# Kernel optimization log

Hardware: AMD Instinct MI355X
Metric: run time of the kernel (lower is better)

## Reference

```python
import jax, jax.numpy as jnp
import numpy as np

D, H = 256, 4            # model dim, num heads
HD = D // H              # head dim (even, needed by rotate_half)
B, N, M, NS = 2, 6, 512, 512  # batch, views, t keypoints, s keypoints
EPS = 1e-5


def _linear(x, w, b):
    return x @ w + b


def _ln(x, g, b):
    mu = x.mean(-1, keepdims=True)
    var = ((x - mu) ** 2).mean(-1, keepdims=True)
    return (x - mu) * jax.lax.rsqrt(var + EPS) * g + b


def _ffn(x, f1w, f1b, lng, lnb, f2w, f2b):
    # Linear(2d,2d) -> LayerNorm -> exact GELU -> Linear(2d,d)
    h = jax.nn.gelu(_ln(_linear(x, f1w, f1b), lng, lnb), approximate=False)
    return _linear(h, f2w, f2b)


def _rotate_half(x):
    # pairs (x0,x1) -> (-x1, x0), interleaved
    return jnp.stack((-x[..., 1::2], x[..., 0::2]), axis=-1).reshape(x.shape)


def _rope(freqs, t):
    return t * freqs[0] + _rotate_half(t) * freqs[1]


def _attn(q, k, v):
    sim = jnp.einsum('...id,...jd->...ij', q, k) * (q.shape[-1] ** -0.5)
    return jnp.einsum('...ij,...jd->...id', jax.nn.softmax(sim, axis=-1), v)


def _self_block(x, enc, qkv_w, qkv_b, out_w, out_b, *ffn_p):
    b, n_img, m, d = x.shape
    enc = jnp.swapaxes(enc, 2, 3)  # encoding.dim()==6 path
    qkv = _linear(x, qkv_w, qkv_b).reshape(b, n_img, m, H, HD, 3)
    qkv = jnp.swapaxes(qkv, -4, -3)  # [b,N,H,m,hd,3]
    q, k, v = qkv[..., 0], qkv[..., 1], qkv[..., 2]
    ctx = _attn(_rope(enc, q), _rope(enc, k), v)  # [b,N,H,m,hd]
    msg = _linear(jnp.swapaxes(ctx, -3, -2).reshape(b, n_img, m, d), out_w, out_b)
    return x + _ffn(jnp.concatenate([x, msg], -1), *ffn_p)


def _t2t_block(t, qkv_w, qkv_b, out_w, out_b, *ffn_p):
    t2 = jnp.swapaxes(t, 1, 2)  # [b,m,N,d]
    b, m, n_img, d = t2.shape
    qkv = _linear(t2, qkv_w, qkv_b).reshape(b, m, n_img, H, HD, 3)
    qkv = jnp.swapaxes(qkv, 3, 2)  # [b,m,H,N,hd,3]
    q, k, v = qkv[..., 0], qkv[..., 1], qkv[..., 2]
    ctx = _attn(q, k, v)  # [b,m,H,N,hd]
    msg = _linear(jnp.swapaxes(ctx, 3, 2).reshape(b, m, n_img, d), out_w, out_b)
    return jnp.swapaxes(t2 + _ffn(jnp.concatenate([t2, msg], -1), *ffn_p), 1, 2)


def _s2s_block(s, q_enc, k_enc, qkv_w, qkv_b, out_w, out_b, *ffn_p):
    b, n_img, n, d = s.shape
    qkv = _linear(s, qkv_w, qkv_b).reshape(b, n_img, n, H, HD, 3)
    qkv = jnp.swapaxes(jnp.swapaxes(qkv, -4, -3), -5, -4)  # [b,H,N,n,hd,3]
    q, k, v = qkv[..., 0], qkv[..., 1], qkv[..., 2]
    # expand queries across all views, RoPE per (i,j) view pair
    q = jnp.broadcast_to(q[:, :, None], (b, H, n_img, n_img, n, HD))
    q = _rope(q_enc, q).reshape(b, H, n_img, n_img * n, HD)
    k = _rope(k_enc, k)
    ctx = _attn(q, k, v).reshape(b, H, n_img, n_img, n, HD)
    # drop diagonal (i==j) entries exactly like boolean-mask indexing in torch
    off = np.nonzero(~np.eye(n_img, dtype=bool).ravel())[0]
    ctx = ctx.reshape(b, H, n_img * n_img, n, HD)[:, :, off]
    ctx = ctx.reshape(b, H, n_img - 1, n_img, n, HD).mean(2)  # [b,H,N,n,hd]
    ctx = jnp.swapaxes(jnp.swapaxes(ctx, 1, 2), 2, 3).reshape(b, n_img, n, d)
    msg = _linear(ctx, out_w, out_b)
    return s + _ffn(jnp.concatenate([s, msg], -1), *ffn_p)


def _cross_block(d0, d1, q_w, q_b, kv_w, kv_b, out_w, out_b, *ffn_p):
    b, n_img, m, d = d0.shape
    m1 = d1.shape[2]
    q = jnp.swapaxes(_linear(d0, q_w, q_b).reshape(b, n_img, m, H, HD), 2, 3)
    kv = jnp.swapaxes(_linear(d1, kv_w, kv_b).reshape(b, n_img, m1, H, HD, 2), 2, 3)
    ctx = _attn(q, kv[..., 0], kv[..., 1])  # [b,N,H,m,hd]
    msg = _linear(jnp.swapaxes(ctx, 2, 3).reshape(b, n_img, m, d), out_w, out_b)
    return d0 + _ffn(jnp.concatenate([d0, msg], -1), *ffn_p)


def setup_inputs() -> dict:
    key = jax.random.key(0)
    ks = iter(jax.random.split(key, 80))
    f32 = jnp.float32

    def lin(din, dout):
        return (jax.random.normal(next(ks), (din, dout), f32) * (din ** -0.5),
                jnp.zeros((dout,), f32))

    inp = {}
    inp['t_desc'] = jax.random.normal(next(ks), (B, N, M, D), f32)
    inp['s_desc'] = jax.random.normal(next(ks), (B, N, NS, D), f32)
    inp['t_encoding'] = jax.random.normal(next(ks), (2, 1, 1, N, M, HD), f32)
    inp['s_encoding'] = jax.random.normal(next(ks), (2, 1, 1, N, NS, HD), f32)
    inp['q_encoding'] = jax.random.normal(next(ks), (2, 1, 1, N, N, 1, HD), f32)
    inp['k_encoding'] = jax.random.normal(next(ks), (2, 1, 1, N, NS, HD), f32)
    for pre in ('sa', 'ss', 'tt'):
        inp[pre + '_qkv_w'], inp[pre + '_qkv_b'] = lin(D, 3 * D)
        inp[pre + '_out_w'], inp[pre + '_out_b'] = lin(D, D)
        inp[pre + '_f1_w'], inp[pre + '_f1_b'] = lin(2 * D, 2 * D)
        inp[pre + '_ln_g'] = jnp.ones((2 * D,), f32)
        inp[pre + '_ln_b'] = jnp.zeros((2 * D,), f32)
        inp[pre + '_f2_w'], inp[pre + '_f2_b'] = lin(2 * D, D)
    inp['ca_q_w'], inp['ca_q_b'] = lin(D, D)
    inp['ca_kv_w'], inp['ca_kv_b'] = lin(D, 2 * D)
    inp['ca_out_w'], inp['ca_out_b'] = lin(D, D)
    inp['ca_f1_w'], inp['ca_f1_b'] = lin(2 * D, 2 * D)
    inp['ca_ln_g'] = jnp.ones((2 * D,), f32)
    inp['ca_ln_b'] = jnp.zeros((2 * D,), f32)
    inp['ca_f2_w'], inp['ca_f2_b'] = lin(2 * D, D)
    inp['cf_w1'], inp['cf_b1'] = lin(D, D)
    inp['cf_w2'], inp['cf_b2'] = lin(D, 1)
    return inp


def reference(t_desc, s_desc, t_encoding, s_encoding, q_encoding, k_encoding,
              sa_qkv_w, sa_qkv_b, sa_out_w, sa_out_b, sa_f1_w, sa_f1_b, sa_ln_g, sa_ln_b, sa_f2_w, sa_f2_b,
              ss_qkv_w, ss_qkv_b, ss_out_w, ss_out_b, ss_f1_w, ss_f1_b, ss_ln_g, ss_ln_b, ss_f2_w, ss_f2_b,
              tt_qkv_w, tt_qkv_b, tt_out_w, tt_out_b, tt_f1_w, tt_f1_b, tt_ln_g, tt_ln_b, tt_f2_w, tt_f2_b,
              ca_q_w, ca_q_b, ca_kv_w, ca_kv_b, ca_out_w, ca_out_b, ca_f1_w, ca_f1_b, ca_ln_g, ca_ln_b, ca_f2_w, ca_f2_b,
              cf_w1, cf_b1, cf_w2, cf_b2):
    sa = (sa_qkv_w, sa_qkv_b, sa_out_w, sa_out_b, sa_f1_w, sa_f1_b, sa_ln_g, sa_ln_b, sa_f2_w, sa_f2_b)
    t = _self_block(t_desc, t_encoding, *sa)   # shared SelfBlock weights
    s = _self_block(s_desc, s_encoding, *sa)
    t = _t2t_block(t, tt_qkv_w, tt_qkv_b, tt_out_w, tt_out_b, tt_f1_w, tt_f1_b, tt_ln_g, tt_ln_b, tt_f2_w, tt_f2_b)
    s = _s2s_block(s, q_encoding, k_encoding, ss_qkv_w, ss_qkv_b, ss_out_w, ss_out_b, ss_f1_w, ss_f1_b, ss_ln_g, ss_ln_b, ss_f2_w, ss_f2_b)
    ca = (ca_q_w, ca_q_b, ca_kv_w, ca_kv_b, ca_out_w, ca_out_b, ca_f1_w, ca_f1_b, ca_ln_g, ca_ln_b, ca_f2_w, ca_f2_b)
    t2 = _cross_block(t, s, *ca)               # shared CrossBlock weights
    s2 = _cross_block(s, t, *ca)
    conf = _linear(jax.nn.relu(_linear(jax.lax.stop_gradient(s), cf_w1, cf_b1)), cf_w2, cf_b2)[..., 0]
    return t2, s2, conf
```

## Files before the change

kernel.cpp:

```cpp
#include <hip/hip_runtime.h>
#include <hip/hip_bf16.h>
#include <math.h>

constexpr int kD   = 256;
constexpr int kH   = 4;
constexpr int kHD  = 64;
constexpr int kB   = 2;
constexpr int kN   = 6;
constexpr int kM   = 512;
constexpr int kRowsH = kB*kN*kM;
constexpr int kRows  = 2*kRowsH;
constexpr int kGrpH  = kB*kN*kH;
constexpr int kGrp   = 2*kGrpH;
constexpr size_t kTOK = (size_t)kRowsH*kD;
constexpr size_t kEncSlab = (size_t)kN*kM*kHD;
constexpr size_t kQEncSlab = (size_t)kN*kN*kHD;
constexpr float kL2E = 1.4426950408889634f;

typedef unsigned short u16;
typedef __attribute__((ext_vector_type(8))) short s16x8;
typedef __attribute__((ext_vector_type(4))) float f32x4;

__device__ __forceinline__ float wred_sum(float v){
  #pragma unroll
  for (int m=32;m>0;m>>=1) v += __shfl_xor(v, m, 64);
  return v;
}
__device__ __forceinline__ u16 f2b(float x){
  union { float f; unsigned u; } a; a.f = x;
  unsigned r = a.u + 0x7fffu + ((a.u >> 16) & 1u);
  return (u16)(r >> 16);
}
__device__ __forceinline__ float b2f(u16 x){
  union { unsigned u; float f; } a; a.u = ((unsigned)x) << 16;
  return a.f;
}
__device__ __forceinline__ unsigned pk2(float lo, float hi){
  union { __hip_bfloat162 h2; unsigned u; } c;
  c.h2 = __float22bfloat162_rn(make_float2(lo, hi));
  return c.u;
}

struct FuseArgs {
  const float* Wout[4]; const float* W1[4];
  const float* bout[4]; const float* b1[4];
  float* Wtmp; float* b1p;
};

__global__ __launch_bounds__(256) void wfuse_k(FuseArgs fa)
{
  const int set = blockIdx.x >> 5;
  const int t = blockIdx.x & 31;
  const int row0 = (t >> 3)*64, col0 = (t & 7)*64;
  const float* A  = fa.Wout[set];
  const float* Bm = fa.W1[set] + 256*512;
  float* C = fa.Wtmp + (size_t)set*(256*512);
  __shared__ float As[16][65];
  __shared__ float Bs[16][64];
  const int tid = threadIdx.x;
  const int tx = tid & 15, ty = tid >> 4;
  const int ar = tid >> 2, ak = (tid & 3)*4;
  const int wr = tid >> 4, wc = (tid & 15)*4;
  float acc[4][4] = {};
  for (int kt = 0; kt < 256; kt += 16) {
    float4 av = *(const float4*)(A + (size_t)(row0+ar)*256 + kt + ak);
    As[ak+0][ar]=av.x; As[ak+1][ar]=av.y; As[ak+2][ar]=av.z; As[ak+3][ar]=av.w;
    *(float4*)(&Bs[wr][wc]) = *(const float4*)(Bm + (size_t)(kt+wr)*512 + col0 + wc);
    __syncthreads();
    #pragma unroll
    for (int k2=0;k2<16;++k2) {
      float a[4], b[4];
      #pragma unroll
      for (int i=0;i<4;++i) a[i]=As[k2][ty*4+i];
      #pragma unroll
      for (int j=0;j<4;++j) b[j]=Bs[k2][tx*4+j];
      #pragma unroll
      for (int i=0;i<4;++i)
        #pragma unroll
        for (int j=0;j<4;++j) acc[i][j] = fmaf(a[i], b[j], acc[i][j]);
    }
    __syncthreads();
  }
  #pragma unroll
  for (int i=0;i<4;++i)
    #pragma unroll
    for (int j=0;j<4;++j)
      C[(size_t)(row0+ty*4+i)*512 + col0+tx*4+j] = acc[i][j];
}

__global__ __launch_bounds__(256) void biasfuse_k(FuseArgs fa)
{
  const int set = blockIdx.x >> 1;
  const int n = (blockIdx.x & 1)*256 + threadIdx.x;
  const float* W1 = fa.W1[set];
  const float* bo = fa.bout[set];
  float s = fa.b1[set][n];
  for (int k = 0; k < 256; ++k)
    s = fmaf(bo[k], W1[(size_t)(256+k)*512 + n], s);
  fa.b1p[set*512 + n] = s;
}

struct WtDesc { const float* W; const float* W2; u16* Wt; int K; int N; int ntiles; };
struct WtTable { WtDesc d[18]; };

__global__ __launch_bounds__(256) void wtcast_k(WtTable tab)
{
  int t = blockIdx.x, mi = 0;
  while (t >= tab.d[mi].ntiles) { t -= tab.d[mi].ntiles; ++mi; }
  const float* W = tab.d[mi].W;
  const float* W2 = tab.d[mi].W2;
  u16* Wt = tab.d[mi].Wt;
  const int K = tab.d[mi].K, N = tab.d[mi].N;
  const int ktn = K >> 5;
  const int nt = t / ktn, kt = t % ktn;
  const int n0 = nt*128, k0 = kt*32;
  u16* dst = Wt + (size_t)t*4096;
  #pragma unroll
  for (int s = 0; s < 2; ++s) {
    const int idx0 = (s*256 + (int)threadIdx.x)*8;
    const int ar = idx0 >> 5;
    const int w8 = (idx0 >> 3) & 3;
    const int sw = (ar >> 1) & 3;
    int kk = k0 + ((w8 ^ sw) << 3);
    const int n  = n0 + ar;
    const float* src = W;
    if (W2 && kk >= 256) { src = W2; kk -= 256; }
    union { u16 u[8]; s16x8 v; } o;
    #pragma unroll
    for (int e = 0; e < 8; ++e)
      o.u[e] = f2b(src[(size_t)(kk + e)*N + n]);
    *(s16x8*)(dst + idx0) = o.v;
  }
}

template<bool A1B, bool A2B, bool CB>
__global__ __launch_bounds__(256) void mmad_k(
    const void* __restrict__ A1a, const void* __restrict__ A1b,
    const void* __restrict__ A2a, const void* __restrict__ A2b, int K1,
    const u16* __restrict__ Wa, const u16* __restrict__ Wb,
    const float* __restrict__ bia, const float* __restrict__ bib,
    const float* __restrict__ bi2a, const float* __restrict__ bi2b, int Ns,
    const float* __restrict__ Ra, const float* __restrict__ Rb,
    void* __restrict__ Cp, int N, int K, int Mh, int doRelu)
{
  __shared__ u16 As[2][128*32];
  __shared__ u16 Bs[2][128*32];
  const int tid = threadIdx.x;
  const int lane = tid & 63, w = tid >> 6;
  const int gx = gridDim.x;
  const int nblk = gx * gridDim.y;
  int flat = blockIdx.y*gx + blockIdx.x;
  if (!(nblk & 7)) flat = (flat & 7)*(nblk >> 3) + (flat >> 3);
  const int bxx = flat % gx, byy = flat / gx;
  const int row0 = byy*128, col0 = bxx*128;
  const bool sec = (row0 >= Mh);
  const int lr0 = sec ? row0 - Mh : row0;
  const void* A1 = sec ? A1b : A1a;
  const void* A2 = sec ? A2b : A2a;
  const u16* Wt  = sec ? Wb : Wa;
  const float* bias  = sec ? bib : bia;
  const float* bias2 = sec ? bi2b : bi2a;
  const float* R = sec ? Rb : Ra;
  const int wr = (w >> 1)*64, wc = (w & 1)*64;
  const int ar = tid >> 1, ah = tid & 1;
  const int K2 = K - K1;
  const int ktn = K >> 5;
  f32x4 acc[4][4] = {};

  auto stage = [&](int buf, int kt) {
    const u16* wtile = Wt + ((size_t)((col0 >> 7)*ktn + (kt >> 5)))*4096;
    #pragma unroll
    for (int s = 0; s < 2; ++s) {
      const u16* srcp = wtile + (size_t)(s*256 + tid)*8;
      __builtin_amdgcn_global_load_lds(
          (const __attribute__((address_space(1))) void*)srcp,
          (__attribute__((address_space(3))) void*)((char*)Bs[buf] + s*4096 + w*1024),
          16, 0, 0);
    }
    const int kk = kt + ah*16;
    union { u16 u[16]; s16x8 v[2]; } tmp;
    if (kk < K1) {
      if constexpr (A1B) {
        const u16* ap = (const u16*)A1 + (size_t)(lr0+ar)*K1 + kk;
        tmp.v[0] = *(const s16x8*)ap; tmp.v[1] = *(const s16x8*)(ap+8);
      } else {
        const float* ap = (const float*)A1 + (size_t)(lr0+ar)*K1 + kk;
        #pragma unroll
        for (int i = 0; i < 16; i += 4) {
          f32x4 v4 = *(const f32x4*)(ap + i);
          tmp.u[i+0]=f2b(v4.x); tmp.u[i+1]=f2b(v4.y); tmp.u[i+2]=f2b(v4.z); tmp.u[i+3]=f2b(v4.w);
        }
      }
    } else {
      if constexpr (A2B) {
        const u16* ap = (const u16*)A2 + (size_t)(lr0+ar)*K2 + (kk - K1);
        tmp.v[0] = *(const s16x8*)ap; tmp.v[1] = *(const s16x8*)(ap+8);
      } else {
        const float* ap = (const float*)A2 + (size_t)(lr0+ar)*K2 + (kk - K1);
        #pragma unroll
        for (int i = 0; i < 16; i += 4) {
          f32x4 v4 = *(const f32x4*)(ap + i);
          tmp.u[i+0]=f2b(v4.x); tmp.u[i+1]=f2b(v4.y); tmp.u[i+2]=f2b(v4.z); tmp.u[i+3]=f2b(v4.w);
        }
      }
    }
    const int sw = (ar >> 1) & 3;
    *(s16x8*)(&As[buf][ar*32 + ((ah*2+0)^sw)*8]) = tmp.v[0];
    *(s16x8*)(&As[buf][ar*32 + ((ah*2+1)^sw)*8]) = tmp.v[1];
  };

  stage(0, 0);
  __syncthreads();
  for (int t = 0; t < ktn; ++t) {
    const int cur = t & 1;
    if (t + 1 < ktn) stage(cur ^ 1, (t + 1) << 5);
    s16x8 af[4], bfv[4];
    #pragma unroll
    for (int fm = 0; fm < 4; ++fm) {
      const int r = wr + fm*16 + (lane & 15);
      const int g = (lane >> 4) ^ ((r >> 1) & 3);
      af[fm] = *(const s16x8*)(&As[cur][r*32 + g*8]);
    }
    #pragma unroll
    for (int fn = 0; fn < 4; ++fn) {
      const int c = wc + fn*16 + (lane & 15);
      const int g = (lane >> 4) ^ ((c >> 1) & 3);
      bfv[fn] = *(const s16x8*)(&Bs[cur][c*32 + g*8]);
    }
    #pragma unroll
    for (int fm = 0; fm < 4; ++fm)
      #pragma unroll
      for (int fn = 0; fn < 4; ++fn)
        acc[fm][fn] = __builtin_amdgcn_mfma_f32_16x16x32_bf16(af[fm], bfv[fn], acc[fm][fn], 0, 0, 0);
    __syncthreads();
  }

  #pragma unroll
  for (int fm = 0; fm < 4; ++fm) {
    const int ro = wr + fm*16 + (lane >> 4)*4;
    #pragma unroll
    for (int fn = 0; fn < 4; ++fn) {
      const int cc = col0 + wc + fn*16 + (lane & 15);
      const float bv = (cc < Ns) ? bias[cc] : bias2[cc - Ns];
      #pragma unroll
      for (int j = 0; j < 4; ++j) {
        float v = acc[fm][fn][j] + bv;
        if (R) v += R[(size_t)(lr0 + ro + j)*N + cc];
        if (doRelu) v = fmaxf(v, 0.f);
        const size_t idx = (size_t)(row0 + ro + j)*N + cc;
        if constexpr (CB) ((u16*)Cp)[idx] = f2b(v);
        else              ((float*)Cp)[idx] = v;
      }
    }
  }
}

__global__ __launch_bounds__(256) void prep_self_k(
    const u16* __restrict__ qkvU, const float* __restrict__ t_enc,
    const float* __restrict__ s_enc,
    u16* __restrict__ Qb, u16* __restrict__ Kb, u16* __restrict__ Vt)
{
  __shared__ u16 vs[64][66];
  const int g = blockIdx.x >> 3, i0 = (blockIdx.x & 7)*64;
  const int h = g & 3, bn = g >> 2;
  const float* enc = (bn < 12) ? t_enc : s_enc;
  const int n = (bn < 12 ? bn : bn - 12) % kN;
  const int c = threadIdx.x & 63, t4 = threadIdx.x >> 6;
  const float sgn = (c & 1) ? 1.f : -1.f;
  #pragma unroll 4
  for (int rr = 0; rr < 16; ++rr) {
    const int il = rr*4 + t4, i = i0 + il;
    const u16* base = qkvU + ((size_t)bn*kM + i)*768 + h*192;
    const float q = b2f(base[c*3]), k = b2f(base[c*3+1]);
    const float qp = b2f(base[(c^1)*3]), kp = b2f(base[(c^1)*3+1]);
    const size_t eo = ((size_t)(n*kM + i))*kHD + c;
    const float e0 = enc[eo], e1 = enc[kEncSlab + eo];
    Qb[((size_t)g*kM + i)*kHD + c] = f2b((q*e0 + sgn*qp*e1)*0.125f);
    Kb[((size_t)g*kM + i)*kHD + c] = f2b(k*e0 + sgn*kp*e1);
    vs[il][c] = base[c*3+2];
  }
  __syncthreads();
  #pragma unroll 4
  for (int rr = 0; rr < 16; ++rr) {
    const int cc = rr*4 + t4;
    Vt[((size_t)g*kHD + cc)*kM + i0 + c] = vs[c][cc];
  }
}

__global__ __launch_bounds__(256) void prep_s2s_k(
    const u16* __restrict__ qkvU, const float* __restrict__ kenc,
    float* __restrict__ Qs, u16* __restrict__ Kb, u16* __restrict__ Vt)
{
  __shared__ u16 vs[64][66];
  const int g = blockIdx.x >> 3, i0 = (blockIdx.x & 7)*64;
  const int view = g % kN, bh = g / kN;
  const int h = bh & 3, b = bh >> 2;
  const int c = threadIdx.x & 63, t4 = threadIdx.x >> 6;
  const float sgn = (c & 1) ? 1.f : -1.f;
  #pragma unroll 4
  for (int rr = 0; rr < 16; ++rr) {
    const int il = rr*4 + t4, i = i0 + il;
    const u16* base = qkvU + ((size_t)(kRowsH + (b*kN+view)*kM + i))*768 + h*192;
    const float k = b2f(base[c*3+1]), kp = b2f(base[(c^1)*3+1]);
    const size_t eo = ((size_t)(view*kM + i))*kHD + c;
    const float e0 = kenc[eo], e1 = kenc[kEncSlab + eo];
    Qs[((size_t)g*kM + i)*kHD + c] = b2f(base[c*3]);
    Kb[((size_t)g*kM + i)*kHD + c] = f2b(k*e0 + sgn*kp*e1);
    vs[il][c] = base[c*3+2];
  }
  __syncthreads();
  #pragma unroll 4
  for (int rr = 0; rr < 16; ++rr) {
    const int cc = rr*4 + t4;
    Vt[((size_t)g*kHD + cc)*kM + i0 + c] = vs[c][cc];
  }
}

__global__ __launch_bounds__(256) void prep_cross_k(
    const u16* __restrict__ qkvC, u16* __restrict__ Kb, u16* __restrict__ Vt)
{
  __shared__ u16 vs[64][66];
  const int g = blockIdx.x >> 3, i0 = (blockIdx.x & 7)*64;
  const int h = g & 3, bn = g >> 2;
  const int src = (bn < 12) ? bn + 12 : bn - 12;
  const int c = threadIdx.x & 63, t4 = threadIdx.x >> 6;
  #pragma unroll 4
  for (int rr = 0; rr < 16; ++rr) {
    const int il = rr*4 + t4, i = i0 + il;
    const u16* base = qkvC + ((size_t)src*kM + i)*768 + 256 + h*128;
    Kb[((size_t)g*kM + i)*kHD + c] = f2b(b2f(base[c*2]) * 0.125f);
    vs[il][c] = base[c*2+1];
  }
  __syncthreads();
  #pragma unroll 4
  for (int rr = 0; rr < 16; ++rr) {
    const int cc = rr*4 + t4;
    Vt[((size_t)g*kHD + cc)*kM + i0 + c] = vs[c][cc];
  }
}

template<int CROSSQ>
__global__ __launch_bounds__(256) void attn_mm_k(
    const u16* __restrict__ Qb, const u16* __restrict__ Kb,
    const u16* __restrict__ Vt, u16* __restrict__ ctx)
{
  const int w = threadIdx.x >> 6, lane = threadIdx.x & 63;
  const int bij = (blockIdx.x & 7)*48 + (blockIdx.x >> 3);
  const int g = bij >> 2, qblk = bij & 3;
  const int h = g & 3, bn = g >> 2;
  const int q0 = qblk*128 + w*32;
  const int qr = lane & 15, hi = lane >> 4;
  const bool subhi = (hi & 1), up = (hi >= 2);

  s16x8 qf0[2], qf1[2];
  #pragma unroll
  for (int f = 0; f < 2; ++f) {
    const u16* qp = CROSSQ
      ? Qb + ((size_t)(bn*kM + q0 + f*16 + qr))*768 + h*kHD + hi*8
      : Qb + ((size_t)g*kM + q0 + f*16 + qr)*kHD + hi*8;
    qf0[f] = *(const s16x8*)(qp);
    qf1[f] = *(const s16x8*)(qp + 32);
  }

  const u16* Kg = Kb + (size_t)g*kM*kHD;
  const u16* Vg = Vt + (size_t)g*kHD*kM;
  f32x4 acc[2][4] = {};
  float m[2] = {-1e30f, -1e30f}, l[2] = {0.f, 0.f};

  s16x8 kA[2][2], kB[2][2];
  f32x4 sA[2][2], sB[2][2];

  auto loadK = [&](s16x8 kb[2][2], int kc){
    #pragma unroll
    for (int t = 0; t < 2; ++t) {
      const u16* kp = Kg + ((size_t)(kc*32 + t*16 + qr))*kHD + hi*8;
      kb[t][0] = *(const s16x8*)(kp);
      kb[t][1] = *(const s16x8*)(kp + 32);
    }
  };
  auto qk = [&](const s16x8 kb[2][2], f32x4 st[2][2]){
    #pragma unroll
    for (int f = 0; f < 2; ++f)
      #pragma unroll
      for (int t = 0; t < 2; ++t) {
        f32x4 z = {0.f, 0.f, 0.f, 0.f};
        z = __builtin_amdgcn_mfma_f32_16x16x32_bf16(kb[t][0], qf0[f], z, 0, 0, 0);
        z = __builtin_amdgcn_mfma_f32_16x16x32_bf16(kb[t][1], qf1[f], z, 0, 0, 0);
        st[f][t] = z;
      }
  };
  auto smpv = [&](f32x4 st[2][2], int kc){
    const int k0 = kc*32;
    s16x8 pa[2];
    #pragma unroll
    for (int f = 0; f < 2; ++f) {
      float mloc = fmaxf(fmaxf(fmaxf(st[f][0][0], st[f][0][1]), fmaxf(st[f][0][2], st[f][0][3])),
                         fmaxf(fmaxf(st[f][1][0], st[f][1][1]), fmaxf(st[f][1][2], st[f][1][3])));
      mloc = fmaxf(mloc, __shfl_xor(mloc, 16));
      mloc = fmaxf(mloc, __shfl_xor(mloc, 32));
      if (!__all(mloc - m[f] <= 8.f)) {
        const float mn = fmaxf(m[f], mloc);
        const float r = exp2f((m[f] - mn)*kL2E);
        m[f] = mn;
        l[f] *= r;
        const float rr0 = __shfl(r, hi*4+0), rr1 = __shfl(r, hi*4+1);
        const float rr2 = __shfl(r, hi*4+2), rr3 = __shfl(r, hi*4+3);
        #pragma unroll
        for (int db = 0; db < 4; ++db) {
          acc[f][db][0] *= rr0; acc[f][db][1] *= rr1;
          acc[f][db][2] *= rr2; acc[f][db][3] *= rr3;
        }
      }
      float p[8], ls = 0.f;
      #pragma unroll
      for (int t = 0; t < 2; ++t)
        #pragma unroll
        for (int j = 0; j < 4; ++j) {
          const float pv = exp2f((st[f][t][j] - m[f])*kL2E);
          p[t*4+j] = pv; ls += pv;
        }
      l[f] += ls;
      const unsigned c00 = pk2(p[0], p[1]);
      const unsigned c01 = pk2(p[2], p[3]);
      const unsigned c10 = pk2(p[4], p[5]);
      const unsigned c11 = pk2(p[6], p[7]);
      const unsigned c00x = __shfl_xor((int)c00, 32), c10x = __shfl_xor((int)c10, 32);
      const unsigned c01x = __shfl_xor((int)c01, 32), c11x = __shfl_xor((int)c11, 32);
      const unsigned E = up ? c10x : c00, F = up ? c10 : c00x;
      const unsigned G = up ? c11x : c01, H = up ? c11 : c01x;
      const unsigned Ex = __shfl_xor((int)E, 16), Fx = __shfl_xor((int)F, 16);
      const unsigned Gx = __shfl_xor((int)G, 16), Hx = __shfl_xor((int)H, 16);
      union { unsigned w[4]; s16x8 v; } pw;
      pw.w[0] = subhi ? Fx : E;
      pw.w[1] = subhi ? Hx : G;
      pw.w[2] = subhi ? F  : Ex;
      pw.w[3] = subhi ? H  : Gx;
      pa[f] = pw.v;
    }
    #pragma unroll
    for (int db = 0; db < 4; ++db) {
      const s16x8 vf = *(const s16x8*)(Vg + ((size_t)(db*16 + qr))*kM + k0 + hi*8);
      acc[0][db] = __builtin_amdgcn_mfma_f32_16x16x32_bf16(pa[0], vf, acc[0][db], 0, 0, 0);
      acc[1][db] = __builtin_amdgcn_mfma_f32_16x16x32_bf16(pa[1], vf, acc[1][db], 0, 0, 0);
    }
  };

  loadK(kA, 0);
  qk(kA, sA);
  loadK(kB, 1);
  for (int kc = 0; kc < 16; kc += 2) {
    qk(kB, sB);
    if (kc + 2 < 16) loadK(kA, kc + 2);
    smpv(sA, kc);
    if (kc + 2 < 16) qk(kA, sA);
    if (kc + 3 < 16) loadK(kB, kc + 3);
    smpv(sB, kc + 1);
  }

  #pragma unroll
  for (int f = 0; f < 2; ++f) {
    float lf = l[f];
    lf += __shfl_xor(lf, 16); lf += __shfl_xor(lf, 32);
    const float li = 1.f/lf;
    const float l0 = __shfl(li, hi*4+0), l1 = __shfl(li, hi*4+1);
    const float l2 = __shfl(li, hi*4+2), l3 = __shfl(li, hi*4+3);
    #pragma unroll
    for (int db = 0; db < 4; ++db) {
      const size_t base = ((size_t)(bn*kM + q0 + f*16 + hi*4))*kD + h*kHD + db*16 + qr;
      ctx[base + 0*kD] = f2b(acc[f][db][0]*l0);
      ctx[base + 1*kD] = f2b(acc[f][db][1]*l1);
      ctx[base + 2*kD] = f2b(acc[f][db][2]*l2);
      ctx[base + 3*kD] = f2b(acc[f][db][3]*l3);
    }
  }
}

__device__ __forceinline__ void rope4(const f32x4 x, const f32x4 e0, const f32x4 e1, float o[4])
{
  o[0] = x[0]*e0[0] - x[1]*e1[0];
  o[1] = x[1]*e0[1] + x[0]*e1[1];
  o[2] = x[2]*e0[2] - x[3]*e1[2];
  o[3] = x[3]*e0[3] + x[2]*e1[3];
}

__global__ __launch_bounds__(256) void attn_s2s_k(
    const float* __restrict__ Qraw, const u16* __restrict__ Kb,
    const u16* __restrict__ Vt, const float* __restrict__ qenc,
    u16* __restrict__ ctx5)
{
  const int w = threadIdx.x >> 6, lane = threadIdx.x & 63;
  const int bij = (blockIdx.x & 7)*120 + (blockIdx.x >> 3);
  const int bh = bij / 120;
  const int rest = bij % 120;
  const int col = rest / 20;
  const int rem = rest % 20;
  const int qblk = rem / 5, split = rem % 5;
  const int q0 = qblk*128 + w*32;
  const int qr = lane & 15, hi = lane >> 4;
  const bool subhi = (hi & 1), up = (hi >= 2);

  const int e  = split*6 + col;
  const int iv = e/5;
  const int j0 = e%5;
  const int jv = j0 + (j0 >= iv ? 1 : 0);

  s16x8 qf0[2], qf1[2];
  #pragma unroll
  for (int f = 0; f < 2; ++f) {
    const float* qp = Qraw + ((size_t)(bh*kN + jv)*kM + q0 + f*16 + qr)*kHD + hi*8;
    const float* ep = qenc + ((size_t)(iv*kN + jv))*kHD + hi*8;
    union { u16 u[8]; s16x8 v; } A, B;
    float o[4];
    rope4(*(const f32x4*)(qp),   *(const f32x4*)(ep),   *(const f32x4*)(ep+kQEncSlab), o);
    #pragma unroll
    for (int j = 0; j < 4; ++j) A.u[j] = f2b(o[j]*0.125f);
    rope4(*(const f32x4*)(qp+4), *(const f32x4*)(ep+4), *(const f32x4*)(ep+kQEncSlab+4), o);
    #pragma unroll
    for (int j = 0; j < 4; ++j) A.u[4+j] = f2b(o[j]*0.125f);
    rope4(*(const f32x4*)(qp+32), *(const f32x4*)(ep+32), *(const f32x4*)(ep+kQEncSlab+32), o);
    #pragma unroll
    for (int j = 0; j < 4; ++j) B.u[j] = f2b(o[j]*0.125f);
    rope4(*(const f32x4*)(qp+36), *(const f32x4*)(ep+36), *(const f32x4*)(ep+kQEncSlab+36), o);
    #pragma unroll
    for (int j = 0; j < 4; ++j) B.u[4+j] = f2b(o[j]*0.125f);
    qf0[f] = A.v; qf1[f] = B.v;
  }

  const int g2 = bh*kN + iv;
  const u16* Kg = Kb + (size_t)g2*kM*kHD;
  const u16* Vg = Vt + (size_t)g2*kHD*kM;
  f32x4 acc[2][4] = {};
  float m[2] = {-1e30f, -1e30f}, l[2] = {0.f, 0.f};

  s16x8 kA[2][2], kB[2][2];
  f32x4 sA[2][2], sB[2][2];

  auto loadK = [&](s16x8 kb[2][2], int kc){
    #pragma unroll
    for (int t = 0; t < 2; ++t) {
      const u16* kp = Kg + ((size_t)(kc*32 + t*16 + qr))*kHD + hi*8;
      kb[t][0] = *(const s16x8*)(kp);
      kb[t][1] = *(const s16x8*)(kp + 32);
    }
  };
  auto qk = [&](const s16x8 kb[2][2], f32x4 st[2][2]){
    #pragma unroll
    for (int f = 0; f < 2; ++f)
      #pragma unroll
      for (int t = 0; t < 2; ++t) {
        f32x4 z = {0.f, 0.f, 0.f, 0.f};
        z = __builtin_amdgcn_mfma_f32_16x16x32_bf16(kb[t][0], qf0[f], z, 0, 0, 0);
        z = __builtin_amdgcn_mfma_f32_16x16x32_bf16(kb[t][1], qf1[f], z, 0, 0, 0);
        st[f][t] = z;
      }
  };
  auto smpv = [&](f32x4 st[2][2], int kc){
    const int k0 = kc*32;
    s16x8 pa[2];
    #pragma unroll
    for (int f = 0; f < 2; ++f) {
      float mloc = fmaxf(fmaxf(fmaxf(st[f][0][0], st[f][0][1]), fmaxf(st[f][0][2], st[f][0][3])),
                         fmaxf(fmaxf(st[f][1][0], st[f][1][1]), fmaxf(st[f][1][2], st[f][1][3])));
      mloc = fmaxf(mloc, __shfl_xor(mloc, 16));
      mloc = fmaxf(mloc, __shfl_xor(mloc, 32));
      if (!__all(mloc - m[f] <= 8.f)) {
        const float mn = fmaxf(m[f], mloc);
        const float r = exp2f((m[f] - mn)*kL2E);
        m[f] = mn;
        l[f] *= r;
        const float rr0 = __shfl(r, hi*4+0), rr1 = __shfl(r, hi*4+1);
        const float rr2 = __shfl(r, hi*4+2), rr3 = __shfl(r, hi*4+3);
        #pragma unroll
        for (int db = 0; db < 4; ++db) {
          acc[f][db][0] *= rr0; acc[f][db][1] *= rr1;
          acc[f][db][2] *= rr2; acc[f][db][3] *= rr3;
        }
      }
      float p[8], ls = 0.f;
      #pragma unroll
      for (int t = 0; t < 2; ++t)
        #pragma unroll
        for (int j = 0; j < 4; ++j) {
          const float pv = exp2f((st[f][t][j] - m[f])*kL2E);
          p[t*4+j] = pv; ls += pv;
        }
      l[f] += ls;
      const unsigned c00 = pk2(p[0], p[1]);
      const unsigned c01 = pk2(p[2], p[3]);
      const unsigned c10 = pk2(p[4], p[5]);
      const unsigned c11 = pk2(p[6], p[7]);
      const unsigned c00x = __shfl_xor((int)c00, 32), c10x = __shfl_xor((int)c10, 32);
      const unsigned c01x = __shfl_xor((int)c01, 32), c11x = __shfl_xor((int)c11, 32);
      const unsigned E = up ? c10x : c00, F = up ? c10 : c00x;
      const unsigned G = up ? c11x : c01, H = up ? c11 : c01x;
      const unsigned Ex = __shfl_xor((int)E, 16), Fx = __shfl_xor((int)F, 16);
      const unsigned Gx = __shfl_xor((int)G, 16), Hx = __shfl_xor((int)H, 16);
      union { unsigned w[4]; s16x8 v; } pw;
      pw.w[0] = subhi ? Fx : E;
      pw.w[1] = subhi ? Hx : G;
      pw.w[2] = subhi ? F  : Ex;
      pw.w[3] = subhi ? H  : Gx;
      pa[f] = pw.v;
    }
    #pragma unroll
    for (int db = 0; db < 4; ++db) {
      const s16x8 vf = *(const s16x8*)(Vg + ((size_t)(db*16 + qr))*kM + k0 + hi*8);
      acc[0][db] = __builtin_amdgcn_mfma_f32_16x16x32_bf16(pa[0], vf, acc[0][db], 0, 0, 0);
      acc[1][db] = __builtin_amdgcn_mfma_f32_16x16x32_bf16(pa[1], vf, acc[1][db], 0, 0, 0);
    }
  };

  loadK(kA, 0);
  qk(kA, sA);
  loadK(kB, 1);
  for (int kc = 0; kc < 16; kc += 2) {
    qk(kB, sB);
    if (kc + 2 < 16) loadK(kA, kc + 2);
    smpv(sA, kc);
    if (kc + 2 < 16) qk(kA, sA);
    if (kc + 3 < 16) loadK(kB, kc + 3);
    smpv(sB, kc + 1);
  }

  const int b = bh >> 2, h = bh & 3;
  u16* outp = ctx5 + (size_t)split*kTOK;
  #pragma unroll
  for (int f = 0; f < 2; ++f) {
    float lf = l[f];
    lf += __shfl_xor(lf, 16); lf += __shfl_xor(lf, 32);
    const float li = 0.2f/lf;
    const float l0 = __shfl(li, hi*4+0), l1 = __shfl(li, hi*4+1);
    const float l2 = __shfl(li, hi*4+2), l3 = __shfl(li, hi*4+3);
    #pragma unroll
    for (int db = 0; db < 4; ++db) {
      const size_t base = ((size_t)((b*kN + col)*kM + q0 + f*16 + hi*4))*kD + h*kHD + db*16 + qr;
      outp[base + 0*kD] = f2b(acc[f][db][0]*l0);
      outp[base + 1*kD] = f2b(acc[f][db][1]*l1);
      outp[base + 2*kD] = f2b(acc[f][db][2]*l2);
      outp[base + 3*kD] = f2b(acc[f][db][3]*l3);
    }
  }
}

__global__ __launch_bounds__(256) void sum5_k(const u16* __restrict__ c5,
                                              u16* __restrict__ outU)
{
  const size_t i4 = ((size_t)blockIdx.x*256 + threadIdx.x)*4;
  float s0=0.f, s1=0.f, s2=0.f, s3=0.f;
  #pragma unroll
  for (int sp = 0; sp < 5; ++sp) {
    uint2 d = *(const uint2*)(c5 + sp*kTOK + i4);
    s0 += b2f((u16)(d.x & 0xffff)); s1 += b2f((u16)(d.x >> 16));
    s2 += b2f((u16)(d.y & 0xffff)); s3 += b2f((u16)(d.y >> 16));
  }
  union { u16 u[4]; uint2 d; } o;
  o.u[0]=f2b(s0); o.u[1]=f2b(s1); o.u[2]=f2b(s2); o.u[3]=f2b(s3);
  *(uint2*)(outU + i4) = o.d;
}

__global__ __launch_bounds__(256) void attn_t2t_k(
    const u16* __restrict__ qkvU, u16* __restrict__ ctxU)
{
  const int wid = blockIdx.x*4 + (threadIdx.x >> 6);
  const int lane = threadIdx.x & 63;
  const int m = wid & 511;
  const int t = wid >> 9;
  const int nq = t % kN;
  const int bh = t / kN;
  const int h = bh & 3, b = bh >> 2;
  const u16* pb[kN];
  #pragma unroll
  for (int nk = 0; nk < kN; ++nk)
    pb[nk] = qkvU + ((size_t)(b*kN+nk)*kM + m)*768 + h*192;
  const float qc = b2f(pb[nq][lane*3]);
  float sim[kN];
  #pragma unroll
  for (int nk = 0; nk < kN; ++nk)
    sim[nk] = wred_sum(qc * b2f(pb[nk][lane*3+1])) * 0.125f;
  float mx = sim[0];
  #pragma unroll
  for (int nk = 1; nk < kN; ++nk) mx = fmaxf(mx, sim[nk]);
  float p[kN], s = 0.f;
  #pragma unroll
  for (int nk = 0; nk < kN; ++nk) { p[nk] = expf(sim[nk]-mx); s += p[nk]; }
  const float inv = 1.f/s;
  float o = 0.f;
  #pragma unroll
  for (int nk = 0; nk < kN; ++nk) o = fmaf(p[nk], b2f(pb[nk][lane*3+2]), o);
  ctxU[((size_t)(b*kN+nq)*kM + m)*kD + h*kHD + lane] = f2b(o*inv);
}

__global__ __launch_bounds__(256) void lngelu_k(
    const float* __restrict__ x, u16* __restrict__ y,
    const float* __restrict__ g0, const float* __restrict__ b0,
    const float* __restrict__ g1, const float* __restrict__ b1, int Mh)
{
  const int row = blockIdx.x;
  const int tid = threadIdx.x;
  const float* g = (row < Mh) ? g0 : g1;
  const float* bb = (row < Mh) ? b0 : b1;
  const float* xr = x + (size_t)row*512;
  const float v0 = xr[tid], v1 = xr[tid+256];
  const int w = tid >> 6, lane = tid & 63;
  __shared__ float red[2][4];
  const float s1 = wred_sum(v0+v1);
  const float s2 = wred_sum(v0*v0+v1*v1);
  if (lane == 0){ red[0][w]=s1; red[1][w]=s2; }
  __syncthreads();
  const float mean = (red[0][0]+red[0][1]+red[0][2]+red[0][3]) * (1.f/512.f);
  const float ms   = (red[1][0]+red[1][1]+red[1][2]+red[1][3]) * (1.f/512.f);
  const float rs = rsqrtf(ms - mean*mean + 1e-5f);
  const float y0 = (v0-mean)*rs*g[tid]     + bb[tid];
  const float y1 = (v1-mean)*rs*g[tid+256] + bb[tid+256];
  y[(size_t)row*512 + tid]     = f2b(0.5f*y0*(1.f+erff(y0*0.70710678118654752f)));
  y[(size_t)row*512 + tid+256] = f2b(0.5f*y1*(1.f+erff(y1*0.70710678118654752f)));
}

__global__ void conf_dot_k(const float* __restrict__ tmp, const float* __restrict__ w2,
                           const float* __restrict__ b2, float* __restrict__ out)
{
  const int w = threadIdx.x >> 6, lane = threadIdx.x & 63;
  const int row = blockIdx.x*4 + w;
  const float* t = tmp + (size_t)row*kD;
  float s = 0.f;
  #pragma unroll
  for (int j=0;j<4;++j) s = fmaf(t[lane+j*64], w2[lane+j*64], s);
  s = wred_sum(s);
  if (lane == 0) out[row] = s + b2[0];
}

extern "C" void kernel_launch(void* const* d_in, const int* in_sizes, int n_in,
                              void* d_out, int out_size, void* d_ws, size_t ws_size,
                              hipStream_t stream)
{
  auto F = [&](int i){ return (const float*)d_in[i]; };
  const float* t_desc = F(0);
  const float* s_desc = F(1);
  const float* t_enc  = F(2);
  const float* s_enc  = F(3);
  const float* q_enc  = F(4);
  const float* k_enc  = F(5);

  char* base = (char*)d_ws;
  float* xts = (float*)base;
  float* xt = xts;
  float* xs = xts + kTOK;
  char* R1  = base + 2*kTOK*sizeof(float);
  char* CTX = R1 + 4*kTOK*sizeof(float);
  char* MSG = CTX + 2*kTOK*sizeof(u16);
  u16* Qb16 = (u16*)(MSG + kTOK*sizeof(float));
  u16* Kb16 = Qb16 + 2*kTOK;
  u16* Vt16 = Kb16 + 2*kTOK;
  u16* wsW  = Vt16 + 2*kTOK;
  u16*   qkvU  = (u16*)R1;
  float* hbuf  = (float*)R1;
  u16*   ctx5  = (u16*)R1;
  float* Wtmp  = (float*)R1;
  u16*   ctxU  = (u16*)CTX;
  float* Qs2s  = (float*)MSG;
  float* confb = (float*)MSG;
  u16*   yU    = (u16*)CTX;

  float* out_t2s2 = (float*)d_out;
  float* out_conf = (float*)d_out + 2*kTOK;

  WtTable tab;
  int nd = 0, total_tiles = 0;
  size_t woff = 0;
  const u16* wp[18];
  auto addw = [&](int idx, const float* W2, int K, int N){
    u16* dst = wsW + woff;
    tab.d[nd] = { F(idx), W2, dst, K, N, (N>>7)*(K>>5) };
    total_tiles += tab.d[nd].ntiles;
    wp[nd] = dst;
    woff += (size_t)K*N;
    ++nd;
    return nd-1;
  };
  const int W_SA_QKV = addw(6,  nullptr, 256, 768);
  const int W_SA_F1  = addw(10, Wtmp + 0*131072, 512, 512);
  const int W_SA_F2  = addw(14, nullptr, 512, 256);
  const int W_SS_QKV = addw(16, nullptr, 256, 768);
  const int W_SS_F1  = addw(20, Wtmp + 1*131072, 512, 512);
  const int W_SS_F2  = addw(24, nullptr, 512, 256);
  const int W_TT_QKV = addw(26, nullptr, 256, 768);
  const int W_TT_F1  = addw(30, Wtmp + 2*131072, 512, 512);
  const int W_TT_F2  = addw(34, nullptr, 512, 256);
  const int W_CA_Q   = addw(36, nullptr, 256, 256);
  const int W_CA_KV  = addw(38, nullptr, 256, 512);
  const int W_CA_F1  = addw(42, Wtmp + 3*131072, 512, 512);
  const int W_CA_F2  = addw(46, nullptr, 512, 256);
  const int W_CF_1   = addw(48, nullptr, 256, 256);
  (void)W_CA_KV;
  float* b1p = (float*)(wsW + woff);

  FuseArgs fa;
  fa.Wout[0]=F(8);  fa.Wout[1]=F(18); fa.Wout[2]=F(28); fa.Wout[3]=F(40);
  fa.W1[0]=F(10);   fa.W1[1]=F(20);   fa.W1[2]=F(30);   fa.W1[3]=F(42);
  fa.bout[0]=F(9);  fa.bout[1]=F(19); fa.bout[2]=F(29); fa.bout[3]=F(41);
  fa.b1[0]=F(11);   fa.b1[1]=F(21);   fa.b1[2]=F(31);   fa.b1[3]=F(43);
  fa.Wtmp = Wtmp; fa.b1p = b1p;
  wfuse_k<<<128, 256, 0, stream>>>(fa);
  biasfuse_k<<<8, 256, 0, stream>>>(fa);
  wtcast_k<<<total_tiles, 256, 0, stream>>>(tab);

  auto mm_f32_to_b16 = [&](const float* a1a, const float* a1b, int wa, int wb2,
                           const float* ba, const float* bb2, u16* c, int N_, int K_){
    dim3 grid(N_/128, kRows/128);
    mmad_k<false,false,true><<<grid,256,0,stream>>>(a1a, a1b, nullptr, nullptr, K_,
        wp[wa], wp[wb2], ba, bb2, ba, bb2, N_, nullptr, nullptr, c, N_, K_, kRowsH, 0);
  };
  auto mm_f1 = [&](const float* a1a, const float* a1b, const u16* a2a, const u16* a2b,
                   int wa, int wb2, const float* ba, const float* bb2, float* c){
    dim3 grid(512/128, kRows/128);
    mmad_k<false,true,false><<<grid,256,0,stream>>>(a1a, a1b, a2a, a2b, 256,
        wp[wa], wp[wb2], ba, bb2, ba, bb2, 512, nullptr, nullptr, c, 512, 512, kRowsH, 0);
  };
  auto mm_f2 = [&](const u16* a1a, const u16* a1b, int wa, int wb2,
                   const float* ba, const float* bb2,
                   const float* ra, const float* rb, float* c){
    dim3 grid(256/128, kRows/128);
    mmad_k<true,false,false><<<grid,256,0,stream>>>(a1a, a1b, nullptr, nullptr, 512,
        wp[wa], wp[wb2], ba, bb2, ba, bb2, 256, ra, rb, c, 256, 512, kRowsH, 0);
  };

  mm_f32_to_b16(t_desc, s_desc, W_SA_QKV, W_SA_QKV, F(7), F(7), qkvU, 768, 256);
  prep_self_k<<<kGrp*8, 256, 0, stream>>>(qkvU, t_enc, s_enc, Qb16, Kb16, Vt16);
  attn_mm_k<0><<<384, 256, 0, stream>>>(Qb16, Kb16, Vt16, ctxU);
  mm_f1(t_desc, s_desc, ctxU, ctxU + kTOK, W_SA_F1, W_SA_F1, b1p+0*512, b1p+0*512, hbuf);
  lngelu_k<<<kRows, 256, 0, stream>>>(hbuf, yU, F(12), F(13), F(12), F(13), kRowsH);
  mm_f2(yU, yU + (size_t)kRowsH*512, W_SA_F2, W_SA_F2, F(15), F(15), t_desc, s_desc, xts);

  mm_f32_to_b16(xt, xs, W_TT_QKV, W_SS_QKV, F(27), F(17), qkvU, 768, 256);
  prep_s2s_k<<<kGrpH*8, 256, 0, stream>>>(qkvU, k_enc, Qs2s, Kb16, Vt16);
  attn_t2t_k<<<(kB*kH*kN*kM)/4, 256, 0, stream>>>(qkvU, ctxU);
  attn_s2s_k<<<960, 256, 0, stream>>>(Qs2s, Kb16, Vt16, q_enc, ctx5);
  sum5_k<<<(int)(kTOK/1024), 256, 0, stream>>>(ctx5, ctxU + kTOK);
  mm_f1(xt, xs, ctxU, ctxU + kTOK, W_TT_F1, W_SS_F1, b1p+2*512, b1p+1*512, hbuf);
  lngelu_k<<<kRows, 256, 0, stream>>>(hbuf, yU, F(32), F(33), F(22), F(23), kRowsH);
  mm_f2(yU, yU + (size_t)kRowsH*512, W_TT_F2, W_SS_F2, F(35), F(25), xt, xs, xts);

  {
    dim3 grid(2, kRowsH/128);
    mmad_k<false,false,false><<<grid,256,0,stream>>>(xs, xs, nullptr, nullptr, 256,
        wp[W_CF_1], wp[W_CF_1], F(49), F(49), F(49), F(49), 256,
        nullptr, nullptr, confb, 256, 256, kRowsH, 1);
  }
  conf_dot_k<<<kRowsH/4, 256, 0, stream>>>(confb, F(50), F(51), out_conf);

  {
    dim3 grid(768/128, kRows/128);
    mmad_k<false,false,true><<<grid,256,0,stream>>>(xt, xs, nullptr, nullptr, 256,
        wp[W_CA_Q], wp[W_CA_Q], F(37), F(37), F(39), F(39), 256,
        nullptr, nullptr, qkvU, 768, 256, kRowsH, 0);
  }
  prep_cross_k<<<kGrp*8, 256, 0, stream>>>(qkvU, Kb16, Vt16);
  attn_mm_k<1><<<384, 256, 0, stream>>>(qkvU, Kb16, Vt16, ctxU);
  mm_f1(xt, xs, ctxU, ctxU + kTOK, W_CA_F1, W_CA_F1, b1p+3*512, b1p+3*512, hbuf);
  lngelu_k<<<kRows, 256, 0, stream>>>(hbuf, yU, F(44), F(45), F(44), F(45), kRowsH);
  mm_f2(yU, yU + (size_t)kRowsH*512, W_CA_F2, W_CA_F2, F(47), F(47), xt, xs, out_t2s2);
}
```

Before: 473.4 us.

## Merge t2t and s2s attention launches, store FFN hidden as bf16, vectorize LN-GELU

Folds the token-to-token attention into the s2s attention kernel as extra blocks, so both run in one launch and the small t2t work can fill idle CUs. The first FFN GEMM now writes its hidden activation as bf16 rather than fp32, which halves that intermediate's write and read traffic. LayerNorm+GELU is rewritten as one row per wavefront with 8-wide vector loads, removing shared memory and block syncs. ctx5 is moved so it no longer aliases the qkv buffer the merged kernel reads. The cost is an extra rounding of pre-LayerNorm values to bf16, which may slightly change accuracy.

```diff
diff --git a/kernel.cpp b/kernel.cpp
--- a/kernel.cpp
+++ b/kernel.cpp
@@ -483,11 +483,42 @@
   o[3] = x[3]*e0[3] + x[2]*e1[3];
 }
 
-__global__ __launch_bounds__(256) void attn_s2s_k(
+__global__ __launch_bounds__(256) void attn_comb_k(
     const float* __restrict__ Qraw, const u16* __restrict__ Kb,
     const u16* __restrict__ Vt, const float* __restrict__ qenc,
-    u16* __restrict__ ctx5)
-{
+    u16* __restrict__ ctx5, const u16* __restrict__ qkvU,
+    u16* __restrict__ ctxU)
+{
+  if (blockIdx.x >= 960) {
+    const int wid = (blockIdx.x - 960)*4 + ((int)threadIdx.x >> 6);
+    const int lane = threadIdx.x & 63;
+    const int mm2 = wid & 511;
+    const int t = wid >> 9;
+    const int nq = t % kN;
+    const int bh2 = t / kN;
+    const int h2 = bh2 & 3, b2 = bh2 >> 2;
+    const u16* pb[kN];
+    #pragma unroll
+    for (int nk = 0; nk < kN; ++nk)
+      pb[nk] = qkvU + ((size_t)(b2*kN+nk)*kM + mm2)*768 + h2*192;
+    const float qc = b2f(pb[nq][lane*3]);
+    float sim[kN];
+    #pragma unroll
+    for (int nk = 0; nk < kN; ++nk)
+      sim[nk] = wred_sum(qc * b2f(pb[nk][lane*3+1])) * 0.125f;
+    float mx = sim[0];
+    #pragma unroll
+    for (int nk = 1; nk < kN; ++nk) mx = fmaxf(mx, sim[nk]);
+    float p[kN], s = 0.f;
+    #pragma unroll
+    for (int nk = 0; nk < kN; ++nk) { p[nk] = expf(sim[nk]-mx); s += p[nk]; }
+    const float inv = 1.f/s;
+    float o = 0.f;
+    #pragma unroll
+    for (int nk = 0; nk < kN; ++nk) o = fmaf(p[nk], b2f(pb[nk][lane*3+2]), o);
+    ctxU[((size_t)(b2*kN+nq)*kM + mm2)*kD + h2*kHD + lane] = f2b(o*inv);
+    return;
+  }
   const int w = threadIdx.x >> 6, lane = threadIdx.x & 63;
   const int bij = (blockIdx.x & 7)*120 + (blockIdx.x >> 3);
   const int bh = bij / 120;
@@ -532,7 +563,7 @@
   f32x4 acc[2][4] = {};
   float m[2] = {-1e30f, -1e30f}, l[2] = {0.f, 0.f};
 
-  s16x8 kA[2][2], kB[2][2];
+  s16x8 kA[2][2], kB2[2][2];
   f32x4 sA[2][2], sB[2][2];
 
   auto loadK = [&](s16x8 kb[2][2], int kc){
@@ -612,13 +643,13 @@
 
   loadK(kA, 0);
   qk(kA, sA);
-  loadK(kB, 1);
+  loadK(kB2, 1);
   for (int kc = 0; kc < 16; kc += 2) {
-    qk(kB, sB);
+    qk(kB2, sB);
     if (kc + 2 < 16) loadK(kA, kc + 2);
     smpv(sA, kc);
     if (kc + 2 < 16) qk(kA, sA);
-    if (kc + 3 < 16) loadK(kB, kc + 3);
+    if (kc + 3 < 16) loadK(kB2, kc + 3);
     smpv(sB, kc + 1);
   }
 
@@ -658,62 +689,40 @@
   *(uint2*)(outU + i4) = o.d;
 }
 
-__global__ __launch_bounds__(256) void attn_t2t_k(
-    const u16* __restrict__ qkvU, u16* __restrict__ ctxU)
-{
-  const int wid = blockIdx.x*4 + (threadIdx.x >> 6);
-  const int lane = threadIdx.x & 63;
-  const int m = wid & 511;
-  const int t = wid >> 9;
-  const int nq = t % kN;
-  const int bh = t / kN;
-  const int h = bh & 3, b = bh >> 2;
-  const u16* pb[kN];
-  #pragma unroll
-  for (int nk = 0; nk < kN; ++nk)
-    pb[nk] = qkvU + ((size_t)(b*kN+nk)*kM + m)*768 + h*192;
-  const float qc = b2f(pb[nq][lane*3]);
-  float sim[kN];
-  #pragma unroll
-  for (int nk = 0; nk < kN; ++nk)
-    sim[nk] = wred_sum(qc * b2f(pb[nk][lane*3+1])) * 0.125f;
-  float mx = sim[0];
-  #pragma unroll
-  for (int nk = 1; nk < kN; ++nk) mx = fmaxf(mx, sim[nk]);
-  float p[kN], s = 0.f;
-  #pragma unroll
-  for (int nk = 0; nk < kN; ++nk) { p[nk] = expf(sim[nk]-mx); s += p[nk]; }
-  const float inv = 1.f/s;
-  float o = 0.f;
-  #pragma unroll
-  for (int nk = 0; nk < kN; ++nk) o = fmaf(p[nk], b2f(pb[nk][lane*3+2]), o);
-  ctxU[((size_t)(b*kN+nq)*kM + m)*kD + h*kHD + lane] = f2b(o*inv);
-}
-
 __global__ __launch_bounds__(256) void lngelu_k(
-    const float* __restrict__ x, u16* __restrict__ y,
+    const u16* __restrict__ x, u16* __restrict__ y,
     const float* __restrict__ g0, const float* __restrict__ b0,
     const float* __restrict__ g1, const float* __restrict__ b1, int Mh)
 {
-  const int row = blockIdx.x;
-  const int tid = threadIdx.x;
+  const int w = threadIdx.x >> 6, lane = threadIdx.x & 63;
+  const int row = blockIdx.x*4 + w;
   const float* g = (row < Mh) ? g0 : g1;
   const float* bb = (row < Mh) ? b0 : b1;
-  const float* xr = x + (size_t)row*512;
-  const float v0 = xr[tid], v1 = xr[tid+256];
-  const int w = tid >> 6, lane = tid & 63;
-  __shared__ float red[2][4];
-  const float s1 = wred_sum(v0+v1);
-  const float s2 = wred_sum(v0*v0+v1*v1);
-  if (lane == 0){ red[0][w]=s1; red[1][w]=s2; }
-  __syncthreads();
-  const float mean = (red[0][0]+red[0][1]+red[0][2]+red[0][3]) * (1.f/512.f);
-  const float ms   = (red[1][0]+red[1][1]+red[1][2]+red[1][3]) * (1.f/512.f);
+  const int o8 = lane*8;
+  union { u16 u[8]; s16x8 v; } xv;
+  xv.v = *(const s16x8*)(x + (size_t)row*512 + o8);
+  float vf[8];
+  float s1 = 0.f, s2 = 0.f;
+  #pragma unroll
+  for (int j = 0; j < 8; ++j) {
+    vf[j] = b2f(xv.u[j]);
+    s1 += vf[j]; s2 += vf[j]*vf[j];
+  }
+  s1 = wred_sum(s1); s2 = wred_sum(s2);
+  const float mean = s1 * (1.f/512.f);
+  const float ms   = s2 * (1.f/512.f);
   const float rs = rsqrtf(ms - mean*mean + 1e-5f);
-  const float y0 = (v0-mean)*rs*g[tid]     + bb[tid];
-  const float y1 = (v1-mean)*rs*g[tid+256] + bb[tid+256];
-  y[(size_t)row*512 + tid]     = f2b(0.5f*y0*(1.f+erff(y0*0.70710678118654752f)));
-  y[(size_t)row*512 + tid+256] = f2b(0.5f*y1*(1.f+erff(y1*0.70710678118654752f)));
+  f32x4 gv0 = *(const f32x4*)(g + o8),  gv1 = *(const f32x4*)(g + o8 + 4);
+  f32x4 bv0 = *(const f32x4*)(bb + o8), bv1 = *(const f32x4*)(bb + o8 + 4);
+  union { u16 u[8]; s16x8 v; } ov;
+  #pragma unroll
+  for (int j = 0; j < 8; ++j) {
+    const float gj = (j < 4) ? gv0[j] : gv1[j-4];
+    const float bj = (j < 4) ? bv0[j] : bv1[j-4];
+    const float yv = (vf[j]-mean)*rs*gj + bj;
+    ov.u[j] = f2b(0.5f*yv*(1.f+erff(yv*0.70710678118654752f)));
+  }
+  *(s16x8*)(y + (size_t)row*512 + o8) = ov.v;
 }
 
 __global__ void conf_dot_k(const float* __restrict__ tmp, const float* __restrict__ w2,
@@ -753,8 +762,8 @@
   u16* Vt16 = Kb16 + 2*kTOK;
   u16* wsW  = Vt16 + 2*kTOK;
   u16*   qkvU  = (u16*)R1;
-  float* hbuf  = (float*)R1;
-  u16*   ctx5  = (u16*)R1;
+  u16*   yH    = (u16*)R1;
+  u16*   ctx5  = qkvU + (size_t)kRowsH*768;
   float* Wtmp  = (float*)R1;
   u16*   ctxU  = (u16*)CTX;
   float* Qs2s  = (float*)MSG;
@@ -811,9 +820,9 @@
         wp[wa], wp[wb2], ba, bb2, ba, bb2, N_, nullptr, nullptr, c, N_, K_, kRowsH, 0);
   };
   auto mm_f1 = [&](const float* a1a, const float* a1b, const u16* a2a, const u16* a2b,
-                   int wa, int wb2, const float* ba, const float* bb2, float* c){
+                   int wa, int wb2, const float* ba, const float* bb2, u16* c){
     dim3 grid(512/128, kRows/128);
-    mmad_k<false,true,false><<<grid,256,0,stream>>>(a1a, a1b, a2a, a2b, 256,
+    mmad_k<false,true,true><<<grid,256,0,stream>>>(a1a, a1b, a2a, a2b, 256,
         wp[wa], wp[wb2], ba, bb2, ba, bb2, 512, nullptr, nullptr, c, 512, 512, kRowsH, 0);
   };
   auto mm_f2 = [&](const u16* a1a, const u16* a1b, int wa, int wb2,
@@ -827,17 +836,16 @@
   mm_f32_to_b16(t_desc, s_desc, W_SA_QKV, W_SA_QKV, F(7), F(7), qkvU, 768, 256);
   prep_self_k<<<kGrp*8, 256, 0, stream>>>(qkvU, t_enc, s_enc, Qb16, Kb16, Vt16);
   attn_mm_k<0><<<384, 256, 0, stream>>>(Qb16, Kb16, Vt16, ctxU);
-  mm_f1(t_desc, s_desc, ctxU, ctxU + kTOK, W_SA_F1, W_SA_F1, b1p+0*512, b1p+0*512, hbuf);
-  lngelu_k<<<kRows, 256, 0, stream>>>(hbuf, yU, F(12), F(13), F(12), F(13), kRowsH);
+  mm_f1(t_desc, s_desc, ctxU, ctxU + kTOK, W_SA_F1, W_SA_F1, b1p+0*512, b1p+0*512, yH);
+  lngelu_k<<<kRows/4, 256, 0, stream>>>(yH, yU, F(12), F(13), F(12), F(13), kRowsH);
   mm_f2(yU, yU + (size_t)kRowsH*512, W_SA_F2, W_SA_F2, F(15), F(15), t_desc, s_desc, xts);
 
   mm_f32_to_b16(xt, xs, W_TT_QKV, W_SS_QKV, F(27), F(17), qkvU, 768, 256);
   prep_s2s_k<<<kGrpH*8, 256, 0, stream>>>(qkvU, k_enc, Qs2s, Kb16, Vt16);
-  attn_t2t_k<<<(kB*kH*kN*kM)/4, 256, 0, stream>>>(qkvU, ctxU);
-  attn_s2s_k<<<960, 256, 0, stream>>>(Qs2s, Kb16, Vt16, q_enc, ctx5);
+  attn_comb_k<<<960 + 6144, 256, 0, stream>>>(Qs2s, Kb16, Vt16, q_enc, ctx5, qkvU, ctxU);
   sum5_k<<<(int)(kTOK/1024), 256, 0, stream>>>(ctx5, ctxU + kTOK);
-  mm_f1(xt, xs, ctxU, ctxU + kTOK, W_TT_F1, W_SS_F1, b1p+2*512, b1p+1*512, hbuf);
-  lngelu_k<<<kRows, 256, 0, stream>>>(hbuf, yU, F(32), F(33), F(22), F(23), kRowsH);
+  mm_f1(xt, xs, ctxU, ctxU + kTOK, W_TT_F1, W_SS_F1, b1p+2*512, b1p+1*512, yH);
+  lngelu_k<<<kRows/4, 256, 0, stream>>>(yH, yU, F(32), F(33), F(22), F(23), kRowsH);
   mm_f2(yU, yU + (size_t)kRowsH*512, W_TT_F2, W_SS_F2, F(35), F(25), xt, xs, xts);
 
   {
@@ -856,7 +864,7 @@
   }
   prep_cross_k<<<kGrp*8, 256, 0, stream>>>(qkvU, Kb16, Vt16);
   attn_mm_k<1><<<384, 256, 0, stream>>>(qkvU, Kb16, Vt16, ctxU);
-  mm_f1(xt, xs, ctxU, ctxU + kTOK, W_CA_F1, W_CA_F1, b1p+3*512, b1p+3*512, hbuf);
-  lngelu_k<<<kRows, 256, 0, stream>>>(hbuf, yU, F(44), F(45), F(44), F(45), kRowsH);
+  mm_f1(xt, xs, ctxU, ctxU + kTOK, W_CA_F1, W_CA_F1, b1p+3*512, b1p+3*512, yH);
+  lngelu_k<<<kRows/4, 256, 0, stream>>>(yH, yU, F(44), F(45), F(44), F(45), kRowsH);
   mm_f2(yU, yU + (size_t)kRowsH*512, W_CA_F2, W_CA_F2, F(47), F(47), xt, xs, out_t2s2);
 }
```

Measured after the change: 470.9 us. About the same (-0.5%).
